# Performance work log

Hardware: AMD Instinct MI355X
Metric: run time of the kernel (lower is better)

## Reference

```python
import jax, jax.numpy as jnp
import numpy as np

N = 50000          # nodes
E = 800000         # edges (before self-loops)
DIN = 1024         # input_dim_mel
HID = 128          # hidden_dim
HEADS = 2
NC = 4             # num_classes
NEG_SLOPE = 0.2    # PyG GATConv default


def setup_inputs() -> dict:
    key = jax.random.key(0)
    ks = jax.random.split(key, 12)
    s = 0.05
    return {
        "x": jax.random.normal(ks[0], (N, DIN), dtype=jnp.float32),
        "edge_index": jax.random.randint(ks[1], (2, E), 0, N, dtype=jnp.int64),
        # linear_pre (stored as [in, out])
        "W_pre": jax.random.normal(ks[2], (DIN, HID), dtype=jnp.float32) * s,
        "b_pre": jnp.zeros((HID,), dtype=jnp.float32),
        # gat1: GATConv(HID, HID, heads=2, concat=True)
        "W1": jax.random.normal(ks[3], (HID, HEADS * HID), dtype=jnp.float32) * s,
        "a_src1": jax.random.normal(ks[4], (HEADS, HID), dtype=jnp.float32) * s,
        "a_dst1": jax.random.normal(ks[5], (HEADS, HID), dtype=jnp.float32) * s,
        "b1": jnp.zeros((HEADS * HID,), dtype=jnp.float32),
        # gat2: GATConv(HID*HEADS, NC, heads=1, concat=True)
        "W2": jax.random.normal(ks[6], (HEADS * HID, NC), dtype=jnp.float32) * s,
        "a_src2": jax.random.normal(ks[7], (1, NC), dtype=jnp.float32) * s,
        "a_dst2": jax.random.normal(ks[8], (1, NC), dtype=jnp.float32) * s,
        "b2": jnp.zeros((NC,), dtype=jnp.float32),
    }


def _gat_conv(x, W, a_src, a_dst, bias, src, dst, heads, out_ch):
    """PyG GATConv (concat=True, self-loops already appended to src/dst)."""
    n = x.shape[0]
    h = (x @ W).reshape(n, heads, out_ch)            # [N,H,C]
    alpha_src = (h * a_src).sum(-1)                  # [N,H]
    alpha_dst = (h * a_dst).sum(-1)                  # [N,H]
    e = alpha_src[src] + alpha_dst[dst]              # [E,H] edge scores
    e = jax.nn.leaky_relu(e, NEG_SLOPE)
    # segment softmax over incoming edges of each dst node
    m = jax.ops.segment_max(e, dst, num_segments=n)  # [N,H]
    e = jnp.exp(e - m[dst])
    s = jax.ops.segment_sum(e, dst, num_segments=n)  # [N,H]
    alpha = e / (s[dst] + 1e-16)                     # [E,H]
    # gather src messages, weight by attention, scatter-add to dst
    out = jax.ops.segment_sum(h[src] * alpha[:, :, None], dst, num_segments=n)
    return out.reshape(n, heads * out_ch) + bias


def reference(x, edge_index, W_pre, b_pre, W1, a_src1, a_dst1, b1,
              W2, a_src2, a_dst2, b2):
    n = x.shape[0]
    # add self-loops (PyG GATConv default)
    loops = jnp.arange(n, dtype=edge_index.dtype)
    src = jnp.concatenate([edge_index[0], loops])
    dst = jnp.concatenate([edge_index[1], loops])

    h = jax.nn.relu(x @ W_pre + b_pre)                               # [N,HID]
    h = jax.nn.elu(_gat_conv(h, W1, a_src1, a_dst1, b1, src, dst, HEADS, HID))
    out = _gat_conv(h, W2, a_src2, a_dst2, b2, src, dst, 1, NC)      # [N,NC]
    return out
```

## Files before the change

kernel.cpp:

```cpp
#include <hip/hip_runtime.h>
#include <hip/hip_bf16.h>

#define NEG_SLOPE 0.2f

typedef __bf16 bf16x8 __attribute__((ext_vector_type(8)));
typedef unsigned short u16x8 __attribute__((ext_vector_type(8)));
typedef float f32x4 __attribute__((ext_vector_type(4)));
typedef unsigned short ushort_t;

#define AS_GLOBAL(p) ((const __attribute__((address_space(1))) void*)(p))
#define AS_SHARED(p) ((__attribute__((address_space(3))) void*)(p))


__global__ void khist(const int* __restrict__ dst, int E, int* __restrict__ counts) {
    int i = blockIdx.x * blockDim.x + threadIdx.x;
    if (i < E) atomicAdd(&counts[dst[i]], 1);
}

__global__ __launch_bounds__(1024) void kscan_part(const int* __restrict__ counts,
                                                   int* __restrict__ row_ptr,
                                                   int* __restrict__ bsum, int n) {
    __shared__ int wsum[16];
    int t = threadIdx.x, lane = t & 63, wid = t >> 6;
    int i = blockIdx.x * 1024 + t;
    int v = (i < n) ? (counts[i] + 1) : 0;
    int x = v;
    #pragma unroll
    for (int off = 1; off < 64; off <<= 1) {
        int y = __shfl_up(x, off, 64);
        if (lane >= off) x += y;
    }
    if (lane == 63) wsum[wid] = x;
    __syncthreads();
    if (wid == 0) {
        int ws = (lane < 16) ? wsum[lane] : 0;
        #pragma unroll
        for (int off = 1; off < 16; off <<= 1) {
            int y = __shfl_up(ws, off, 64);
            if (lane >= off) ws += y;
        }
        if (lane < 16) wsum[lane] = ws;
    }
    __syncthreads();
    int wave_excl = (wid == 0) ? 0 : wsum[wid - 1];
    if (i < n) row_ptr[i] = wave_excl + (x - v);
    if (t == 0) bsum[blockIdx.x] = wsum[15];
}

__global__ void kscan_tops(const int* __restrict__ bsum, int* __restrict__ boff,
                           int* __restrict__ row_ptr, int G, int n) {
    int lane = threadIdx.x;
    int v = (lane < G) ? bsum[lane] : 0;
    int x = v;
    #pragma unroll
    for (int off = 1; off < 64; off <<= 1) {
        int y = __shfl_up(x, off, 64);
        if (lane >= off) x += y;
    }
    if (lane < G) boff[lane] = x - v;
    if (lane == 63) row_ptr[n] = x;
}

__global__ void kscan_add(int* __restrict__ row_ptr, const int* __restrict__ boff,
                          int* __restrict__ cursor, int n) {
    int i = blockIdx.x * blockDim.x + threadIdx.x;
    if (i < n) {
        int r = row_ptr[i] + boff[i >> 10];
        row_ptr[i] = r;
        cursor[i] = r;
    }
}

__global__ void kfill(const int* __restrict__ src, const int* __restrict__ dst,
                      int E, int n, int* __restrict__ cursor, int* __restrict__ edge_src) {
    int i = blockIdx.x * blockDim.x + threadIdx.x;
    if (i < E) {
        int p = atomicAdd(&cursor[dst[i]], 1);
        edge_src[p] = src[i];
    } else if (i < E + n) {
        int v = i - E;
        int p = atomicAdd(&cursor[v], 1);
        edge_src[p] = v;
    }
}

__global__ void kprep(const float* __restrict__ Wpre, const float* __restrict__ W1,
                      ushort_t* __restrict__ PreH, ushort_t* __restrict__ PreL,
                      ushort_t* __restrict__ W1H, ushort_t* __restrict__ W1L) {
    int i = blockIdx.x * blockDim.x + threadIdx.x;
    if (i < 1024 * 128) {
        int k = i >> 7, n = i & 127;
        float f = Wpre[i];
        unsigned u = __float_as_uint(f);
        float lf = f - __uint_as_float(u & 0xffff0000u);
        int d = ((k >> 3) * 128 + n) * 8 + (k & 7);
        PreH[d] = (ushort_t)(u >> 16);
        PreL[d] = (ushort_t)(__float_as_uint(lf) >> 16);
    } else if (i < 1024 * 128 + 128 * 256) {
        int j2 = i - 1024 * 128;
        int k = j2 >> 8, n = j2 & 255;
        float f = W1[j2];
        unsigned u = __float_as_uint(f);
        float lf = f - __uint_as_float(u & 0xffff0000u);
        int d = ((k >> 3) * 256 + n) * 8 + (k & 7);
        W1H[d] = (ushort_t)(u >> 16);
        W1L[d] = (ushort_t)(__float_as_uint(lf) >> 16);
    }
}

__device__ inline void split8(const float* v, bf16x8& hi, bf16x8& lo) {
    u16x8 h, l;
    #pragma unroll
    for (int i = 0; i < 8; ++i) {
        unsigned u = __float_as_uint(v[i]);
        h[i] = (ushort_t)(u >> 16);
        float lf = v[i] - __uint_as_float(u & 0xffff0000u);
        l[i] = (ushort_t)(__float_as_uint(lf) >> 16);
    }
    hi = __builtin_bit_cast(bf16x8, h);
    lo = __builtin_bit_cast(bf16x8, l);
}

__global__ __launch_bounds__(256) void kgemm_mfma1(const float* __restrict__ A,
                                                   const ushort_t* __restrict__ Bhi,
                                                   const ushort_t* __restrict__ Blo,
                                                   const float* __restrict__ bias,
                                                   float* __restrict__ C, int M) {
    __shared__ __align__(16) ushort_t Bs[16384];
    int t = threadIdx.x;
    int wid = t >> 6, lane = t & 63;
    int q = lane >> 4, l15 = lane & 15;
    int m0 = blockIdx.x * 64 + wid * 16;
    int m = m0 + l15;
    const float* arow = A + (size_t)(m < M ? m : 0) * 1024;

    f32x4 acc[8];
    #pragma unroll
    for (int c = 0; c < 8; ++c) acc[c] = (f32x4){0.f, 0.f, 0.f, 0.f};

    float4 av[2][4];
    #pragma unroll
    for (int ks = 0; ks < 2; ++ks) {
        av[0][ks * 2]     = *(const float4*)(arow + ks * 32 + q * 8);
        av[0][ks * 2 + 1] = *(const float4*)(arow + ks * 32 + q * 8 + 4);
    }

    #pragma unroll 2
    for (int kt = 0; kt < 16; ++kt) {
        int cur = kt & 1, nxt = cur ^ 1;
        __syncthreads();
        {
            const ushort_t* sH = Bhi + kt * 8192;
            const ushort_t* sL = Blo + kt * 8192;
            #pragma unroll
            for (int i = 0; i < 4; ++i) {
                int ge = (i * 256 + t) * 8;
                int le = (i * 256 + (t & 0xC0)) * 8;
                __builtin_amdgcn_global_load_lds(AS_GLOBAL(sH + ge), AS_SHARED(Bs + le), 16, 0, 0);
                __builtin_amdgcn_global_load_lds(AS_GLOBAL(sL + ge), AS_SHARED(Bs + 8192 + le), 16, 0, 0);
            }
        }
        if (kt < 15) {
            const float* a2 = arow + (kt + 1) * 64;
            #pragma unroll
            for (int ks = 0; ks < 2; ++ks) {
                av[nxt][ks * 2]     = *(const float4*)(a2 + ks * 32 + q * 8);
                av[nxt][ks * 2 + 1] = *(const float4*)(a2 + ks * 32 + q * 8 + 4);
            }
        }
        __syncthreads();
        #pragma unroll
        for (int ks = 0; ks < 2; ++ks) {
            bf16x8 ah, al;
            split8((const float*)&av[cur][ks * 2], ah, al);
            int kc = ks * 4 + q;
            #pragma unroll
            for (int c = 0; c < 8; ++c) {
                int off = (kc * 128 + c * 16 + l15) * 8;
                bf16x8 bh = *(const bf16x8*)(Bs + off);
                bf16x8 bl = *(const bf16x8*)(Bs + 8192 + off);
                acc[c] = __builtin_amdgcn_mfma_f32_16x16x32_bf16(ah, bh, acc[c], 0, 0, 0);
                acc[c] = __builtin_amdgcn_mfma_f32_16x16x32_bf16(al, bh, acc[c], 0, 0, 0);
                acc[c] = __builtin_amdgcn_mfma_f32_16x16x32_bf16(ah, bl, acc[c], 0, 0, 0);
            }
        }
    }
    #pragma unroll
    for (int c = 0; c < 8; ++c) {
        int n = c * 16 + l15;
        float bv = bias[n];
        #pragma unroll
        for (int r = 0; r < 4; ++r) {
            int mm = m0 + q * 4 + r;
            if (mm < M) C[(size_t)mm * 128 + n] = fmaxf(acc[c][r] + bv, 0.f);
        }
    }
}

__global__ __launch_bounds__(256) void kgemm_mfma2(const float* __restrict__ A,
                                                   const ushort_t* __restrict__ Bhi,
                                                   const ushort_t* __restrict__ Blo,
                                                   ushort_t* __restrict__ C, int M) {
    __shared__ __align__(16) ushort_t Bs[32768];
    int t = threadIdx.x;
    int wid = t >> 6, lane = t & 63;
    int q = lane >> 4, l15 = lane & 15;
    int g = blockIdx.y;
    int m0 = blockIdx.x * 64 + wid * 16;
    int m = m0 + l15;
    const float* arow = A + (size_t)(m < M ? m : 0) * 128;

    {
        #pragma unroll
        for (int i = 0; i < 8; ++i) {
            int j = i * 4 + wid;
            int kc = j >> 1, h1k = j & 1;
            int ge = ((kc * 256) + g * 128 + h1k * 64 + lane) * 8;
            int le = j * 512;
            __builtin_amdgcn_global_load_lds(AS_GLOBAL(Bhi + ge), AS_SHARED(Bs + le), 16, 0, 0);
            __builtin_amdgcn_global_load_lds(AS_GLOBAL(Blo + ge), AS_SHARED(Bs + 16384 + le), 16, 0, 0);
        }
    }
    float av[32];
    #pragma unroll
    for (int ks = 0; ks < 4; ++ks) {
        *(float4*)&av[ks * 8 + 0] = *(const float4*)(arow + ks * 32 + q * 8);
        *(float4*)&av[ks * 8 + 4] = *(const float4*)(arow + ks * 32 + q * 8 + 4);
    }
    __syncthreads();

    f32x4 acc[8];
    #pragma unroll
    for (int c = 0; c < 8; ++c) acc[c] = (f32x4){0.f, 0.f, 0.f, 0.f};

    #pragma unroll
    for (int ks = 0; ks < 4; ++ks) {
        bf16x8 ah, al;
        split8(&av[ks * 8], ah, al);
        int kc = ks * 4 + q;
        #pragma unroll
        for (int c = 0; c < 8; ++c) {
            int off = (kc * 128 + c * 16 + l15) * 8;
            bf16x8 bh = *(const bf16x8*)(Bs + off);
            bf16x8 bl = *(const bf16x8*)(Bs + 16384 + off);
            acc[c] = __builtin_amdgcn_mfma_f32_16x16x32_bf16(ah, bh, acc[c], 0, 0, 0);
            acc[c] = __builtin_amdgcn_mfma_f32_16x16x32_bf16(al, bh, acc[c], 0, 0, 0);
            acc[c] = __builtin_amdgcn_mfma_f32_16x16x32_bf16(ah, bl, acc[c], 0, 0, 0);
        }
    }
    #pragma unroll
    for (int c = 0; c < 8; ++c) {
        int n = g * 128 + c * 16 + l15;
        #pragma unroll
        for (int r = 0; r < 4; ++r) {
            int mm = m0 + q * 4 + r;
            if (mm < M) {
                unsigned u = __float_as_uint(acc[c][r]);
                unsigned b = (u + 0x7fffu + ((u >> 16) & 1u)) >> 16;
                C[(size_t)mm * 256 + n] = (ushort_t)b;
            }
        }
    }
}

__global__ __launch_bounds__(256) void kalpha1(const ushort_t* __restrict__ h1b,
                                               const float* __restrict__ a_src,
                                               const float* __restrict__ a_dst,
                                               float* __restrict__ as1,
                                               float* __restrict__ ad1, int n) {
    int wid = threadIdx.x >> 6, lane = threadIdx.x & 63;
    int node = blockIdx.x * 4 + wid;
    if (node >= n) return;
    uint2 p = *(const uint2*)(h1b + (size_t)node * 256 + lane * 4);
    float h0 = __uint_as_float(p.x << 16);
    float h1v = __uint_as_float(p.x & 0xffff0000u);
    float h2v = __uint_as_float(p.y << 16);
    float h3 = __uint_as_float(p.y & 0xffff0000u);
    float4 sv = ((const float4*)a_src)[lane];
    float4 dv = ((const float4*)a_dst)[lane];
    float ps = h0 * sv.x + h1v * sv.y + h2v * sv.z + h3 * sv.w;
    float pd = h0 * dv.x + h1v * dv.y + h2v * dv.z + h3 * dv.w;
    #pragma unroll
    for (int off = 16; off >= 1; off >>= 1) {
        ps += __shfl_down(ps, off, 32);
        pd += __shfl_down(pd, off, 32);
    }
    if ((lane & 31) == 0) {
        int h = lane >> 5;
        as1[node * 2 + h] = ps;
        ad1[node * 2 + h] = pd;
    }
}

__global__ __launch_bounds__(128) void kagg1(const ushort_t* __restrict__ h1b,
                                             const float* __restrict__ as1,
                                             const float* __restrict__ ad1,
                                             const float* __restrict__ b1,
                                             const int* __restrict__ row_ptr,
                                             const int* __restrict__ edge_src,
                                             float* __restrict__ out1, int n) {
    __shared__ float w_lds[128];
    __shared__ int   s_lds[64];
    int node = blockIdx.x;
    int t = threadIdx.x;
    int beg = row_ptr[node], end = row_ptr[node + 1];
    int h_ch = t >> 6;
    float adv = ad1[node * 2 + (t & 1)];
    float acc0 = 0.f, acc1 = 0.f, ssum = 0.f;
    for (int base = beg; base < end; base += 64) {
        int cnt = min(64, end - base);
        int i = t >> 1, h = t & 1;
        if (i < cnt) {
            int s = edge_src[base + i];
            float e = as1[s * 2 + h] + adv;
            e = (e > 0.f) ? e : NEG_SLOPE * e;
            w_lds[i * 2 + h] = __expf(e);
            if (h == 0) s_lds[i] = s;
        }
        __syncthreads();
        #pragma unroll 4
        for (int i2 = 0; i2 < cnt; ++i2) {
            float wv = w_lds[i2 * 2 + h_ch];
            int s = s_lds[i2];
            unsigned p = *(const unsigned*)(h1b + (size_t)s * 256 + t * 2);
            acc0 += wv * __uint_as_float(p << 16);
            acc1 += wv * __uint_as_float(p & 0xffff0000u);
            ssum += wv;
        }
        __syncthreads();
    }
    float inv = 1.f / (ssum + 1e-16f);
    float o0 = acc0 * inv + b1[t * 2];
    float o1 = acc1 * inv + b1[t * 2 + 1];
    o0 = (o0 > 0.f) ? o0 : (__expf(o0) - 1.f);
    o1 = (o1 > 0.f) ? o1 : (__expf(o1) - 1.f);
    *(float2*)(out1 + (size_t)node * 256 + t * 2) = make_float2(o0, o1);
}

__global__ __launch_bounds__(256) void klin2(const float* __restrict__ out1,
                                             const float* __restrict__ W2,
                                             const float* __restrict__ a_src2,
                                             const float* __restrict__ a_dst2,
                                             float* __restrict__ h2,
                                             float* __restrict__ as2,
                                             float* __restrict__ ad2, int n) {
    int wid = threadIdx.x >> 6, lane = threadIdx.x & 63;
    int node = blockIdx.x * 4 + wid;
    if (node >= n) return;
    float4 r = ((const float4*)(out1 + (size_t)node * 256))[lane];
    const float* w = W2 + lane * 16;
    float4 w0 = *(const float4*)(w + 0);
    float4 w1 = *(const float4*)(w + 4);
    float4 w2v = *(const float4*)(w + 8);
    float4 w3 = *(const float4*)(w + 12);
    float a0 = r.x * w0.x + r.y * w1.x + r.z * w2v.x + r.w * w3.x;
    float a1 = r.x * w0.y + r.y * w1.y + r.z * w2v.y + r.w * w3.y;
    float a2 = r.x * w0.z + r.y * w1.z + r.z * w2v.z + r.w * w3.z;
    float a3 = r.x * w0.w + r.y * w1.w + r.z * w2v.w + r.w * w3.w;
    #pragma unroll
    for (int off = 32; off >= 1; off >>= 1) {
        a0 += __shfl_down(a0, off);
        a1 += __shfl_down(a1, off);
        a2 += __shfl_down(a2, off);
        a3 += __shfl_down(a3, off);
    }
    if (lane == 0) {
        h2[node * 4 + 0] = a0; h2[node * 4 + 1] = a1;
        h2[node * 4 + 2] = a2; h2[node * 4 + 3] = a3;
        as2[node] = a0 * a_src2[0] + a1 * a_src2[1] + a2 * a_src2[2] + a3 * a_src2[3];
        ad2[node] = a0 * a_dst2[0] + a1 * a_dst2[1] + a2 * a_dst2[2] + a3 * a_dst2[3];
    }
}

__global__ __launch_bounds__(256) void kagg2(const float* __restrict__ h2,
                                             const float* __restrict__ as2,
                                             const float* __restrict__ ad2,
                                             const float* __restrict__ b2,
                                             const int* __restrict__ row_ptr,
                                             const int* __restrict__ edge_src,
                                             float* __restrict__ out, int n) {
    int wid = threadIdx.x >> 6, lane = threadIdx.x & 63;
    int node = blockIdx.x * 4 + wid;
    if (node >= n) return;
    int beg = row_ptr[node], end = row_ptr[node + 1];
    int j = lane & 3, ig = lane >> 2;
    float adv = ad2[node];
    float acc = 0.f, ssum = 0.f;
    for (int p = beg + ig; p < end; p += 16) {
        int s = edge_src[p];
        float e = as2[s] + adv;
        e = (e > 0.f) ? e : NEG_SLOPE * e;
        float wv = __expf(e);
        acc += wv * h2[s * 4 + j];
        ssum += wv;
    }
    #pragma unroll
    for (int off = 32; off >= 4; off >>= 1) {
        acc += __shfl_down(acc, off);
        ssum += __shfl_down(ssum, off);
    }
    if (lane < 4) out[node * 4 + j] = acc / (ssum + 1e-16f) + b2[j];
}

extern "C" void kernel_launch(void* const* d_in, const int* in_sizes, int n_in,
                              void* d_out, int out_size, void* d_ws, size_t ws_size,
                              hipStream_t stream) {
    const float* x      = (const float*)d_in[0];
    const int*   ei     = (const int*)d_in[1];
    const float* W_pre  = (const float*)d_in[2];
    const float* b_pre  = (const float*)d_in[3];
    const float* W1     = (const float*)d_in[4];
    const float* a_src1 = (const float*)d_in[5];
    const float* a_dst1 = (const float*)d_in[6];
    const float* b1     = (const float*)d_in[7];
    const float* W2     = (const float*)d_in[8];
    const float* a_src2 = (const float*)d_in[9];
    const float* a_dst2 = (const float*)d_in[10];
    const float* b2     = (const float*)d_in[11];
    float* out = (float*)d_out;

    const int DIN = 1024;
    const int E = in_sizes[1] / 2;
    const int N = in_sizes[0] / DIN;

    const int* esrc = ei;
    const int* edst = ei + E;

    char* ws = (char*)d_ws;
    size_t off = 0;
    ushort_t* h1b = (ushort_t*)(ws + off); off += (size_t)N * 256 * 2;
    float* h0 = (float*)(ws + off);
    float* out1 = h0;                 off += (size_t)N * 256 * 4;
    float* as1 = (float*)(ws + off);  off += (size_t)N * 2 * 4;
    float* ad1 = (float*)(ws + off);  off += (size_t)N * 2 * 4;
    float* h2  = (float*)(ws + off);  off += (size_t)N * 4 * 4;
    float* as2 = (float*)(ws + off);  off += (size_t)N * 4;
    float* ad2 = (float*)(ws + off);  off += (size_t)N * 4;
    int* row_ptr = (int*)(ws + off);  off += ((size_t)N + 16) * 4;
    int* cursor  = (int*)(ws + off);  off += (size_t)N * 4;
    int* counts  = (int*)(ws + off);  off += (size_t)N * 4;
    int* bsum    = (int*)(ws + off);  off += 64 * 4;
    int* boff    = (int*)(ws + off);  off += 64 * 4;
    int* edge_src = (int*)(ws + off); off += (size_t)(E + N) * 4;
    ushort_t* PreH = (ushort_t*)(ws + off); off += 1024 * 128 * 2;
    ushort_t* PreL = (ushort_t*)(ws + off); off += 1024 * 128 * 2;
    ushort_t* W1H  = (ushort_t*)(ws + off); off += 128 * 256 * 2;
    ushort_t* W1L  = (ushort_t*)(ws + off); off += 128 * 256 * 2;

    int G = (N + 1023) / 1024;

    kprep<<<640, 256, 0, stream>>>(W_pre, W1, PreH, PreL, W1H, W1L);
    hipMemsetAsync(counts, 0, (size_t)N * 4, stream);
    khist<<<(E + 255) / 256, 256, 0, stream>>>(edst, E, counts);
    kscan_part<<<G, 1024, 0, stream>>>(counts, row_ptr, bsum, N);
    kscan_tops<<<1, 64, 0, stream>>>(bsum, boff, row_ptr, G, N);
    kscan_add<<<(N + 255) / 256, 256, 0, stream>>>(row_ptr, boff, cursor, N);
    kfill<<<(E + N + 255) / 256, 256, 0, stream>>>(esrc, edst, E, N, cursor, edge_src);

    int Mb = (N + 63) / 64;
    kgemm_mfma1<<<Mb, 256, 0, stream>>>(x, PreH, PreL, b_pre, h0, N);
    {
        dim3 grid(Mb, 2);
        kgemm_mfma2<<<grid, 256, 0, stream>>>(h0, W1H, W1L, h1b, N);
    }
    kalpha1<<<(N + 3) / 4, 256, 0, stream>>>(h1b, a_src1, a_dst1, as1, ad1, N);
    kagg1<<<N, 128, 0, stream>>>(h1b, as1, ad1, b1, row_ptr, edge_src, out1, N);
    klin2<<<(N + 3) / 4, 256, 0, stream>>>(out1, W2, a_src2, a_dst2, h2, as2, ad2, N);
    kagg2<<<(N + 3) / 4, 256, 0, stream>>>(h2, as2, ad2, b2, row_ptr, edge_src, out, N);
}
```

Baseline: 558.5 us.

## Fuse alpha and second linear into GEMM/aggregation, use bf16 intermediates

Stores the first-layer activations as bf16 and runs the second GEMM as a single bf16 MFMA pass instead of the three-pass hi/lo split. The attention logit computation is fused into the GEMM epilogue, and the layer-2 linear plus its attention logits are fused into the layer-1 aggregation kernel. This removes two kernel launches and the fp32 round trips of h0 and out1 through memory. The cost is lower precision in the hidden activations and W1, plus an extra block-level reduction with a barrier in kagg1.

```diff
diff --git a/kernel.cpp b/kernel.cpp
--- a/kernel.cpp
+++ b/kernel.cpp
@@ -10,6 +10,11 @@
 
 #define AS_GLOBAL(p) ((const __attribute__((address_space(1))) void*)(p))
 #define AS_SHARED(p) ((__attribute__((address_space(3))) void*)(p))
+
+__device__ inline ushort_t rne_bf16(float f) {
+    unsigned u = __float_as_uint(f);
+    return (ushort_t)((u + 0x7fffu + ((u >> 16) & 1u)) >> 16);
+}
 
 
 __global__ void khist(const int* __restrict__ dst, int E, int* __restrict__ counts) {
@@ -86,7 +91,7 @@
 
 __global__ void kprep(const float* __restrict__ Wpre, const float* __restrict__ W1,
                       ushort_t* __restrict__ PreH, ushort_t* __restrict__ PreL,
-                      ushort_t* __restrict__ W1H, ushort_t* __restrict__ W1L) {
+                      ushort_t* __restrict__ W1b) {
     int i = blockIdx.x * blockDim.x + threadIdx.x;
     if (i < 1024 * 128) {
         int k = i >> 7, n = i & 127;
@@ -99,12 +104,8 @@
     } else if (i < 1024 * 128 + 128 * 256) {
         int j2 = i - 1024 * 128;
         int k = j2 >> 8, n = j2 & 255;
-        float f = W1[j2];
-        unsigned u = __float_as_uint(f);
-        float lf = f - __uint_as_float(u & 0xffff0000u);
         int d = ((k >> 3) * 256 + n) * 8 + (k & 7);
-        W1H[d] = (ushort_t)(u >> 16);
-        W1L[d] = (ushort_t)(__float_as_uint(lf) >> 16);
+        W1b[d] = rne_bf16(W1[j2]);
     }
 }
 
@@ -125,7 +126,7 @@
                                                    const ushort_t* __restrict__ Bhi,
                                                    const ushort_t* __restrict__ Blo,
                                                    const float* __restrict__ bias,
-                                                   float* __restrict__ C, int M) {
+                                                   ushort_t* __restrict__ C, int M) {
     __shared__ __align__(16) ushort_t Bs[16384];
     int t = threadIdx.x;
     int wid = t >> 6, lane = t & 63;
@@ -192,60 +193,54 @@
         #pragma unroll
         for (int r = 0; r < 4; ++r) {
             int mm = m0 + q * 4 + r;
-            if (mm < M) C[(size_t)mm * 128 + n] = fmaxf(acc[c][r] + bv, 0.f);
-        }
-    }
-}
-
-__global__ __launch_bounds__(256) void kgemm_mfma2(const float* __restrict__ A,
-                                                   const ushort_t* __restrict__ Bhi,
-                                                   const ushort_t* __restrict__ Blo,
-                                                   ushort_t* __restrict__ C, int M) {
-    __shared__ __align__(16) ushort_t Bs[32768];
+            if (mm < M) C[(size_t)mm * 128 + n] = rne_bf16(fmaxf(acc[c][r] + bv, 0.f));
+        }
+    }
+}
+
+__global__ __launch_bounds__(256) void kgemm_mfma2(const ushort_t* __restrict__ Ab,
+                                                   const ushort_t* __restrict__ W1b,
+                                                   const float* __restrict__ a_src,
+                                                   const float* __restrict__ a_dst,
+                                                   ushort_t* __restrict__ C,
+                                                   float* __restrict__ as1,
+                                                   float* __restrict__ ad1, int M) {
+    __shared__ __align__(16) ushort_t Bs[16384];
     int t = threadIdx.x;
     int wid = t >> 6, lane = t & 63;
     int q = lane >> 4, l15 = lane & 15;
     int g = blockIdx.y;
     int m0 = blockIdx.x * 64 + wid * 16;
     int m = m0 + l15;
-    const float* arow = A + (size_t)(m < M ? m : 0) * 128;
+    const ushort_t* arow = Ab + (size_t)(m < M ? m : 0) * 128;
 
     {
         #pragma unroll
         for (int i = 0; i < 8; ++i) {
             int j = i * 4 + wid;
-            int kc = j >> 1, h1k = j & 1;
-            int ge = ((kc * 256) + g * 128 + h1k * 64 + lane) * 8;
+            int kc = j >> 1, hk = j & 1;
+            int ge = ((kc * 256) + g * 128 + hk * 64 + lane) * 8;
             int le = j * 512;
-            __builtin_amdgcn_global_load_lds(AS_GLOBAL(Bhi + ge), AS_SHARED(Bs + le), 16, 0, 0);
-            __builtin_amdgcn_global_load_lds(AS_GLOBAL(Blo + ge), AS_SHARED(Bs + 16384 + le), 16, 0, 0);
-        }
-    }
-    float av[32];
+            __builtin_amdgcn_global_load_lds(AS_GLOBAL(W1b + ge), AS_SHARED(Bs + le), 16, 0, 0);
+        }
+    }
+    bf16x8 af[4];
+    #pragma unroll
+    for (int ks = 0; ks < 4; ++ks)
+        af[ks] = *(const bf16x8*)(arow + ks * 32 + q * 8);
+    __syncthreads();
+
+    f32x4 acc[8];
+    #pragma unroll
+    for (int c = 0; c < 8; ++c) acc[c] = (f32x4){0.f, 0.f, 0.f, 0.f};
+
     #pragma unroll
     for (int ks = 0; ks < 4; ++ks) {
-        *(float4*)&av[ks * 8 + 0] = *(const float4*)(arow + ks * 32 + q * 8);
-        *(float4*)&av[ks * 8 + 4] = *(const float4*)(arow + ks * 32 + q * 8 + 4);
-    }
-    __syncthreads();
-
-    f32x4 acc[8];
-    #pragma unroll
-    for (int c = 0; c < 8; ++c) acc[c] = (f32x4){0.f, 0.f, 0.f, 0.f};
-
-    #pragma unroll
-    for (int ks = 0; ks < 4; ++ks) {
-        bf16x8 ah, al;
-        split8(&av[ks * 8], ah, al);
         int kc = ks * 4 + q;
         #pragma unroll
         for (int c = 0; c < 8; ++c) {
-            int off = (kc * 128 + c * 16 + l15) * 8;
-            bf16x8 bh = *(const bf16x8*)(Bs + off);
-            bf16x8 bl = *(const bf16x8*)(Bs + 16384 + off);
-            acc[c] = __builtin_amdgcn_mfma_f32_16x16x32_bf16(ah, bh, acc[c], 0, 0, 0);
-            acc[c] = __builtin_amdgcn_mfma_f32_16x16x32_bf16(al, bh, acc[c], 0, 0, 0);
-            acc[c] = __builtin_amdgcn_mfma_f32_16x16x32_bf16(ah, bl, acc[c], 0, 0, 0);
+            bf16x8 b = *(const bf16x8*)(Bs + (kc * 128 + c * 16 + l15) * 8);
+            acc[c] = __builtin_amdgcn_mfma_f32_16x16x32_bf16(af[ks], b, acc[c], 0, 0, 0);
         }
     }
     #pragma unroll
@@ -254,41 +249,38 @@
         #pragma unroll
         for (int r = 0; r < 4; ++r) {
             int mm = m0 + q * 4 + r;
-            if (mm < M) {
-                unsigned u = __float_as_uint(acc[c][r]);
-                unsigned b = (u + 0x7fffu + ((u >> 16) & 1u)) >> 16;
-                C[(size_t)mm * 256 + n] = (ushort_t)b;
+            if (mm < M) C[(size_t)mm * 256 + n] = rne_bf16(acc[c][r]);
+        }
+    }
+    float asv[4] = {0.f, 0.f, 0.f, 0.f};
+    float adv[4] = {0.f, 0.f, 0.f, 0.f};
+    #pragma unroll
+    for (int c = 0; c < 8; ++c) {
+        float sa = a_src[g * 128 + c * 16 + l15];
+        float da = a_dst[g * 128 + c * 16 + l15];
+        #pragma unroll
+        for (int r = 0; r < 4; ++r) {
+            asv[r] += acc[c][r] * sa;
+            adv[r] += acc[c][r] * da;
+        }
+    }
+    #pragma unroll
+    for (int off = 1; off <= 8; off <<= 1) {
+        #pragma unroll
+        for (int r = 0; r < 4; ++r) {
+            asv[r] += __shfl_xor(asv[r], off, 64);
+            adv[r] += __shfl_xor(adv[r], off, 64);
+        }
+    }
+    if (l15 == 0) {
+        #pragma unroll
+        for (int r = 0; r < 4; ++r) {
+            int node = m0 + q * 4 + r;
+            if (node < M) {
+                as1[node * 2 + g] = asv[r];
+                ad1[node * 2 + g] = adv[r];
             }
         }
-    }
-}
-
-__global__ __launch_bounds__(256) void kalpha1(const ushort_t* __restrict__ h1b,
-                                               const float* __restrict__ a_src,
-                                               const float* __restrict__ a_dst,
-                                               float* __restrict__ as1,
-                                               float* __restrict__ ad1, int n) {
-    int wid = threadIdx.x >> 6, lane = threadIdx.x & 63;
-    int node = blockIdx.x * 4 + wid;
-    if (node >= n) return;
-    uint2 p = *(const uint2*)(h1b + (size_t)node * 256 + lane * 4);
-    float h0 = __uint_as_float(p.x << 16);
-    float h1v = __uint_as_float(p.x & 0xffff0000u);
-    float h2v = __uint_as_float(p.y << 16);
-    float h3 = __uint_as_float(p.y & 0xffff0000u);
-    float4 sv = ((const float4*)a_src)[lane];
-    float4 dv = ((const float4*)a_dst)[lane];
-    float ps = h0 * sv.x + h1v * sv.y + h2v * sv.z + h3 * sv.w;
-    float pd = h0 * dv.x + h1v * dv.y + h2v * dv.z + h3 * dv.w;
-    #pragma unroll
-    for (int off = 16; off >= 1; off >>= 1) {
-        ps += __shfl_down(ps, off, 32);
-        pd += __shfl_down(pd, off, 32);
-    }
-    if ((lane & 31) == 0) {
-        int h = lane >> 5;
-        as1[node * 2 + h] = ps;
-        ad1[node * 2 + h] = pd;
     }
 }
 
@@ -296,23 +288,30 @@
                                              const float* __restrict__ as1,
                                              const float* __restrict__ ad1,
                                              const float* __restrict__ b1,
+                                             const float* __restrict__ W2,
+                                             const float* __restrict__ a_src2,
+                                             const float* __restrict__ a_dst2,
                                              const int* __restrict__ row_ptr,
                                              const int* __restrict__ edge_src,
-                                             float* __restrict__ out1, int n) {
+                                             float* __restrict__ h2,
+                                             float* __restrict__ as2,
+                                             float* __restrict__ ad2, int n) {
     __shared__ float w_lds[128];
     __shared__ int   s_lds[64];
+    __shared__ float red[2][4];
     int node = blockIdx.x;
     int t = threadIdx.x;
+    int wid = t >> 6;
     int beg = row_ptr[node], end = row_ptr[node + 1];
     int h_ch = t >> 6;
-    float adv = ad1[node * 2 + (t & 1)];
+    float advv = ad1[node * 2 + (t & 1)];
     float acc0 = 0.f, acc1 = 0.f, ssum = 0.f;
     for (int base = beg; base < end; base += 64) {
         int cnt = min(64, end - base);
         int i = t >> 1, h = t & 1;
         if (i < cnt) {
             int s = edge_src[base + i];
-            float e = as1[s * 2 + h] + adv;
+            float e = as1[s * 2 + h] + advv;
             e = (e > 0.f) ? e : NEG_SLOPE * e;
             w_lds[i * 2 + h] = __expf(e);
             if (h == 0) s_lds[i] = s;
@@ -334,41 +333,34 @@
     float o1 = acc1 * inv + b1[t * 2 + 1];
     o0 = (o0 > 0.f) ? o0 : (__expf(o0) - 1.f);
     o1 = (o1 > 0.f) ? o1 : (__expf(o1) - 1.f);
-    *(float2*)(out1 + (size_t)node * 256 + t * 2) = make_float2(o0, o1);
-}
-
-__global__ __launch_bounds__(256) void klin2(const float* __restrict__ out1,
-                                             const float* __restrict__ W2,
-                                             const float* __restrict__ a_src2,
-                                             const float* __restrict__ a_dst2,
-                                             float* __restrict__ h2,
-                                             float* __restrict__ as2,
-                                             float* __restrict__ ad2, int n) {
-    int wid = threadIdx.x >> 6, lane = threadIdx.x & 63;
-    int node = blockIdx.x * 4 + wid;
-    if (node >= n) return;
-    float4 r = ((const float4*)(out1 + (size_t)node * 256))[lane];
-    const float* w = W2 + lane * 16;
-    float4 w0 = *(const float4*)(w + 0);
-    float4 w1 = *(const float4*)(w + 4);
-    float4 w2v = *(const float4*)(w + 8);
-    float4 w3 = *(const float4*)(w + 12);
-    float a0 = r.x * w0.x + r.y * w1.x + r.z * w2v.x + r.w * w3.x;
-    float a1 = r.x * w0.y + r.y * w1.y + r.z * w2v.y + r.w * w3.y;
-    float a2 = r.x * w0.z + r.y * w1.z + r.z * w2v.z + r.w * w3.z;
-    float a3 = r.x * w0.w + r.y * w1.w + r.z * w2v.w + r.w * w3.w;
-    #pragma unroll
-    for (int off = 32; off >= 1; off >>= 1) {
-        a0 += __shfl_down(a0, off);
-        a1 += __shfl_down(a1, off);
-        a2 += __shfl_down(a2, off);
-        a3 += __shfl_down(a3, off);
-    }
-    if (lane == 0) {
-        h2[node * 4 + 0] = a0; h2[node * 4 + 1] = a1;
-        h2[node * 4 + 2] = a2; h2[node * 4 + 3] = a3;
-        as2[node] = a0 * a_src2[0] + a1 * a_src2[1] + a2 * a_src2[2] + a3 * a_src2[3];
-        ad2[node] = a0 * a_dst2[0] + a1 * a_dst2[1] + a2 * a_dst2[2] + a3 * a_dst2[3];
+    float4 w0 = *(const float4*)(W2 + t * 8);
+    float4 w1 = *(const float4*)(W2 + t * 8 + 4);
+    float p0 = o0 * w0.x + o1 * w1.x;
+    float p1 = o0 * w0.y + o1 * w1.y;
+    float p2 = o0 * w0.z + o1 * w1.z;
+    float p3 = o0 * w0.w + o1 * w1.w;
+    #pragma unroll
+    for (int off = 1; off < 64; off <<= 1) {
+        p0 += __shfl_xor(p0, off, 64);
+        p1 += __shfl_xor(p1, off, 64);
+        p2 += __shfl_xor(p2, off, 64);
+        p3 += __shfl_xor(p3, off, 64);
+    }
+    if ((t & 63) == 0) {
+        red[wid][0] = p0; red[wid][1] = p1; red[wid][2] = p2; red[wid][3] = p3;
+    }
+    __syncthreads();
+    if (t == 0) {
+        float hv[4], s2 = 0.f, d2 = 0.f;
+        #pragma unroll
+        for (int j = 0; j < 4; ++j) {
+            hv[j] = red[0][j] + red[1][j];
+            h2[node * 4 + j] = hv[j];
+            s2 += hv[j] * a_src2[j];
+            d2 += hv[j] * a_dst2[j];
+        }
+        as2[node] = s2;
+        ad2[node] = d2;
     }
 }
 
@@ -429,8 +421,7 @@
     char* ws = (char*)d_ws;
     size_t off = 0;
     ushort_t* h1b = (ushort_t*)(ws + off); off += (size_t)N * 256 * 2;
-    float* h0 = (float*)(ws + off);
-    float* out1 = h0;                 off += (size_t)N * 256 * 4;
+    ushort_t* h0b = (ushort_t*)(ws + off); off += (size_t)N * 128 * 2;
     float* as1 = (float*)(ws + off);  off += (size_t)N * 2 * 4;
     float* ad1 = (float*)(ws + off);  off += (size_t)N * 2 * 4;
     float* h2  = (float*)(ws + off);  off += (size_t)N * 4 * 4;
@@ -444,12 +435,11 @@
     int* edge_src = (int*)(ws + off); off += (size_t)(E + N) * 4;
     ushort_t* PreH = (ushort_t*)(ws + off); off += 1024 * 128 * 2;
     ushort_t* PreL = (ushort_t*)(ws + off); off += 1024 * 128 * 2;
-    ushort_t* W1H  = (ushort_t*)(ws + off); off += 128 * 256 * 2;
-    ushort_t* W1L  = (ushort_t*)(ws + off); off += 128 * 256 * 2;
+    ushort_t* W1b  = (ushort_t*)(ws + off); off += 128 * 256 * 2;
 
     int G = (N + 1023) / 1024;
 
-    kprep<<<640, 256, 0, stream>>>(W_pre, W1, PreH, PreL, W1H, W1L);
+    kprep<<<640, 256, 0, stream>>>(W_pre, W1, PreH, PreL, W1b);
     hipMemsetAsync(counts, 0, (size_t)N * 4, stream);
     khist<<<(E + 255) / 256, 256, 0, stream>>>(edst, E, counts);
     kscan_part<<<G, 1024, 0, stream>>>(counts, row_ptr, bsum, N);
@@ -458,13 +448,12 @@
     kfill<<<(E + N + 255) / 256, 256, 0, stream>>>(esrc, edst, E, N, cursor, edge_src);
 
     int Mb = (N + 63) / 64;
-    kgemm_mfma1<<<Mb, 256, 0, stream>>>(x, PreH, PreL, b_pre, h0, N);
+    kgemm_mfma1<<<Mb, 256, 0, stream>>>(x, PreH, PreL, b_pre, h0b, N);
     {
         dim3 grid(Mb, 2);
-        kgemm_mfma2<<<grid, 256, 0, stream>>>(h0, W1H, W1L, h1b, N);
-    }
-    kalpha1<<<(N + 3) / 4, 256, 0, stream>>>(h1b, a_src1, a_dst1, as1, ad1, N);
-    kagg1<<<N, 128, 0, stream>>>(h1b, as1, ad1, b1, row_ptr, edge_src, out1, N);
-    klin2<<<(N + 3) / 4, 256, 0, stream>>>(out1, W2, a_src2, a_dst2, h2, as2, ad2, N);
+        kgemm_mfma2<<<grid, 256, 0, stream>>>(h0b, W1b, a_src1, a_dst1, h1b, as1, ad1, N);
+    }
+    kagg1<<<N, 128, 0, stream>>>(h1b, as1, ad1, b1, W2, a_src2, a_dst2,
+                                 row_ptr, edge_src, h2, as2, ad2, N);
     kagg2<<<(N + 3) / 4, 256, 0, stream>>>(h2, as2, ad2, b2, row_ptr, edge_src, out, N);
 }
```

Result: faster. 532.3 us (-4.7%).
